# Performance work log

Hardware: AMD Instinct MI355X
Metric: run time of the kernel (lower is better)

Reference implementation:

```python
import jax, jax.numpy as jnp
import numpy as np

N_NODES = 50000
N_EDGES = 600000
N_GRAPHS = 128
D = 128
L = 3
OUT = 10
BN_EPS = 1e-5


def setup_inputs() -> dict:
    key = jax.random.key(0)
    ks = jax.random.split(key, 8)
    x = jax.random.normal(ks[0], (N_NODES, D), dtype=jnp.float32)
    edge_index = jax.random.randint(ks[1], (2, N_EDGES), 0, N_NODES, dtype=jnp.int64)
    batch = jnp.sort(jax.random.randint(ks[2], (N_NODES,), 0, N_GRAPHS, dtype=jnp.int64))
    s = 0.05
    return {
        "x": x,
        "edge_index": edge_index,
        "batch": batch,
        "convW1": jax.random.normal(ks[3], (L, D, D), dtype=jnp.float32) * s,
        "convb1": jnp.zeros((L, D), dtype=jnp.float32),
        "convg": jnp.ones((L, D), dtype=jnp.float32),
        "convbt": jnp.zeros((L, D), dtype=jnp.float32),
        "convW2": jax.random.normal(ks[4], (L, D, D), dtype=jnp.float32) * s,
        "convb2": jnp.zeros((L, D), dtype=jnp.float32),
        "mW1": jax.random.normal(ks[5], (D, D), dtype=jnp.float32) * s,
        "mb1": jnp.zeros((D,), dtype=jnp.float32),
        "mg": jnp.ones((D,), dtype=jnp.float32),
        "mbt": jnp.zeros((D,), dtype=jnp.float32),
        "mW2": jax.random.normal(ks[6], (D, OUT), dtype=jnp.float32) * s,
        "mb2": jnp.zeros((OUT,), dtype=jnp.float32),
    }


def _mlp(h, W1, b1, g, bt, W2, b2):
    # PyG MLP: Linear -> BatchNorm(eval: mean=0, var=1) -> ReLU -> Linear (plain last)
    inv = 1.0 / jnp.sqrt(1.0 + BN_EPS)
    h = h @ W1 + b1
    h = jnp.maximum(h * (inv * g) + bt, 0.0)
    return h @ W2 + b2


def reference(x, edge_index, batch, convW1, convb1, convg, convbt, convW2, convb2,
              mW1, mb1, mg, mbt, mW2, mb2):
    src, dst = edge_index[0], edge_index[1]
    for l in range(L):
        # GINConv (eps=0): nn(x + scatter-add of neighbor features)
        agg = jax.ops.segment_sum(x[src], dst, num_segments=N_NODES)  # [N, D]
        x = _mlp(x + agg, convW1[l], convb1[l], convg[l], convbt[l], convW2[l], convb2[l])
        x = jnp.maximum(x, 0.0)  # .relu() after conv
    pooled = jax.ops.segment_sum(x, batch, num_segments=N_GRAPHS)  # [G, D]
    return _mlp(pooled, mW1, mb1, mg, mbt, mW2, mb2)  # [G, OUT]
```

## Files before the change

### kernel.cpp

```cpp
#include <hip/hip_runtime.h>

#define N_NODES 50000
#define N_EDGES 600000
#define N_GRAPHS 128
#define DIM 128
#define NLAYERS 3
#define NOUT 10
#define ELLW 48
#define LSTRIDE 136
#define ZROW N_NODES

typedef unsigned short u16;
typedef __attribute__((ext_vector_type(8))) short bf16x8;
typedef __attribute__((ext_vector_type(4))) float f32x4;

__device__ __forceinline__ float bf2f(u16 v) {
    unsigned u = ((unsigned)v) << 16;
    return __builtin_bit_cast(float, u);
}
__device__ __forceinline__ u16 f2bf(float f) {
    unsigned u = __builtin_bit_cast(unsigned, f);
    u = u + 0x7fffu + ((u >> 16) & 1u);
    return (u16)(u >> 16);
}

__global__ void zero_small(int* __restrict__ deg, float* __restrict__ pooled) {
    int i = blockIdx.x * blockDim.x + threadIdx.x;
    if (i < N_NODES) deg[i] = 0;
    if (i < N_GRAPHS * DIM) pooled[i] = 0.f;
}

__global__ void prep_all(int* __restrict__ deg, int* __restrict__ ell,
                         const int* __restrict__ srcs, const int* __restrict__ dsts,
                         u16* __restrict__ xb, u16* __restrict__ bufA, u16* __restrict__ bufB,
                         const float* __restrict__ x, u16* __restrict__ Wswz,
                         const float* __restrict__ convW1, const float* __restrict__ convW2) {
    int i = blockIdx.x * blockDim.x + threadIdx.x;
    if (i < N_EDGES) {
        int d = dsts[i];
        int slot = atomicAdd(&deg[d], 1);
        if (slot < ELLW) ell[(size_t)d * ELLW + slot] = srcs[i];
    }
    if (i < DIM) {
        xb[(size_t)ZROW * DIM + i] = 0;
        bufA[(size_t)ZROW * DIM + i] = 0;
        bufB[(size_t)ZROW * DIM + i] = 0;
    }
    if (i < 6 * 16384) {
        int j = i & 7, lane = (i >> 3) & 63, cb = (i >> 9) & 7, kc = (i >> 12) & 3, w = i >> 14;
        int k = kc * 32 + ((lane >> 4) << 3) + j;
        int c = (cb << 4) + (lane & 15);
        const float* W = (w < 3) ? (convW1 + (size_t)w * 16384) : (convW2 + (size_t)(w - 3) * 16384);
        Wswz[i] = f2bf(W[k * DIM + c]);
    }
    if (i < N_NODES * DIM / 4) {
        float4 v = ((const float4*)x)[i];
        ushort4 o;
        o.x = f2bf(v.x); o.y = f2bf(v.y); o.z = f2bf(v.z); o.w = f2bf(v.w);
        ((ushort4*)xb)[i] = o;
    }
}

__global__ __launch_bounds__(256) void layer_fused(
    u16* __restrict__ out, const u16* __restrict__ x,
    const int* __restrict__ deg, const int* __restrict__ ell,
    const u16* __restrict__ W1f, const u16* __restrict__ W2f,
    const float* __restrict__ b1, const float* __restrict__ g1,
    const float* __restrict__ bt1, const float* __restrict__ b2) {
    __shared__ u16 A[16 * LSTRIDE];
    __shared__ u16 H[16 * LSTRIDE];
    const int tid = threadIdx.x;
    const int wv = tid >> 6;
    const int lane = tid & 63;
    const int row0 = blockIdx.x * 16;

    const size_t coff = (size_t)lane * 2;
    {
        const int r0 = wv << 2;
        int len[4];
        const int* ep[4];
        float ax[4], ay[4];
#pragma unroll
        for (int r = 0; r < 4; ++r) {
            const int grow = row0 + r0 + r;
            len[r] = min(deg[grow], ELLW);
            ep[r] = ell + (size_t)grow * ELLW;
            ushort2 self = *(const ushort2*)(x + (size_t)grow * DIM + coff);
            ax[r] = bf2f(self.x);
            ay[r] = bf2f(self.y);
        }
        const int maxlen = max(max(len[0], len[1]), max(len[2], len[3]));
        for (int j = 0; j < maxlen; j += 4) {
            int id[4][4];
#pragma unroll
            for (int r = 0; r < 4; ++r) {
                int4 e = *(const int4*)(ep[r] + j);
                id[r][0] = (j + 0 < len[r]) ? e.x : ZROW;
                id[r][1] = (j + 1 < len[r]) ? e.y : ZROW;
                id[r][2] = (j + 2 < len[r]) ? e.z : ZROW;
                id[r][3] = (j + 3 < len[r]) ? e.w : ZROW;
            }
#pragma unroll
            for (int r = 0; r < 4; ++r) {
                float px = 0.f, py = 0.f;
#pragma unroll
                for (int t = 0; t < 4; ++t) {
                    ushort2 v = *(const ushort2*)(x + (size_t)id[r][t] * DIM + coff);
                    px += bf2f(v.x);
                    py += bf2f(v.y);
                }
                ax[r] += px;
                ay[r] += py;
            }
        }
#pragma unroll
        for (int r = 0; r < 4; ++r) {
            ushort2 o;
            o.x = f2bf(ax[r]);
            o.y = f2bf(ay[r]);
            *(ushort2*)&A[(r0 + r) * LSTRIDE + lane * 2] = o;
        }
    }
    __syncthreads();

    const float inv = rsqrtf(1.f + 1e-5f);
    const int col0 = lane & 15;
    const int rbl = (lane >> 4) << 2;
    const int fragoff = (lane & 15) * LSTRIDE + ((lane >> 4) << 3);

    {
        f32x4 acc[2];
        acc[0] = (f32x4){0.f, 0.f, 0.f, 0.f};
        acc[1] = (f32x4){0.f, 0.f, 0.f, 0.f};
#pragma unroll
        for (int kc = 0; kc < 4; ++kc) {
            bf16x8 a = *(const bf16x8*)&A[fragoff + kc * 32];
#pragma unroll
            for (int m = 0; m < 2; ++m) {
                const int cb = (wv << 1) + m;
                bf16x8 bb = *(const bf16x8*)(W1f + ((((kc << 3) + cb) << 6 | lane) << 3));
                acc[m] = __builtin_amdgcn_mfma_f32_16x16x32_bf16(a, bb, acc[m], 0, 0, 0);
            }
        }
#pragma unroll
        for (int m = 0; m < 2; ++m) {
            const int c = (((wv << 1) + m) << 4) + col0;
            const float bias = b1[c];
            const float sg = inv * g1[c];
            const float st = bt1[c];
#pragma unroll
            for (int q = 0; q < 4; ++q) {
                float v = (acc[m][q] + bias) * sg + st;
                H[(rbl + q) * LSTRIDE + c] = f2bf(fmaxf(v, 0.f));
            }
        }
    }
    __syncthreads();

    {
        f32x4 acc[2];
        acc[0] = (f32x4){0.f, 0.f, 0.f, 0.f};
        acc[1] = (f32x4){0.f, 0.f, 0.f, 0.f};
#pragma unroll
        for (int kc = 0; kc < 4; ++kc) {
            bf16x8 a = *(const bf16x8*)&H[fragoff + kc * 32];
#pragma unroll
            for (int m = 0; m < 2; ++m) {
                const int cb = (wv << 1) + m;
                bf16x8 bb = *(const bf16x8*)(W2f + ((((kc << 3) + cb) << 6 | lane) << 3));
                acc[m] = __builtin_amdgcn_mfma_f32_16x16x32_bf16(a, bb, acc[m], 0, 0, 0);
            }
        }
#pragma unroll
        for (int m = 0; m < 2; ++m) {
            const int c = (((wv << 1) + m) << 4) + col0;
            const float bias = b2[c];
#pragma unroll
            for (int q = 0; q < 4; ++q) {
                float v = acc[m][q] + bias;
                A[(rbl + q) * LSTRIDE + c] = f2bf(fmaxf(v, 0.f));
            }
        }
    }
    __syncthreads();

    {
        const int r = tid >> 4;
        const int seg = tid & 15;
        uint4 v = *(const uint4*)&A[r * LSTRIDE + seg * 8];
        *(uint4*)(out + (size_t)(row0 + r) * DIM + seg * 8) = v;
    }
}

__global__ __launch_bounds__(256) void pool_partial(float* __restrict__ pooled,
                                                    const u16* __restrict__ x,
                                                    const int* __restrict__ batch) {
    const int chunk = (blockIdx.x * 256 + threadIdx.x) >> 6;
    const int lane = threadIdx.x & 63;
    const int beg = chunk * 16;
    if (beg >= N_NODES) return;
    const int end = min(beg + 16, N_NODES);
    const size_t coff = (size_t)lane * 2;

    float ax = 0.f, ay = 0.f;
    int curg = batch[beg];
    for (int n = beg; n < end; ++n) {
        int g = batch[n];
        if (g != curg) {
            atomicAdd(&pooled[(size_t)curg * DIM + coff], ax);
            atomicAdd(&pooled[(size_t)curg * DIM + coff + 1], ay);
            ax = 0.f; ay = 0.f; curg = g;
        }
        ushort2 v = *(const ushort2*)(x + (size_t)n * DIM + coff);
        ax += bf2f(v.x);
        ay += bf2f(v.y);
    }
    atomicAdd(&pooled[(size_t)curg * DIM + coff], ax);
    atomicAdd(&pooled[(size_t)curg * DIM + coff + 1], ay);
}

__global__ __launch_bounds__(128) void tail_mlp(float* __restrict__ out,
                                                const float* __restrict__ pooled,
                                                const float* __restrict__ mW1,
                                                const float* __restrict__ mb1,
                                                const float* __restrict__ mg,
                                                const float* __restrict__ mbt,
                                                const float* __restrict__ mW2,
                                                const float* __restrict__ mb2) {
    const int g = blockIdx.x;
    const int c = threadIdx.x;
    __shared__ float pl[DIM];
    __shared__ float hd[DIM];
    pl[c] = pooled[(size_t)g * DIM + c];
    __syncthreads();

    float s = 0.f;
#pragma unroll 4
    for (int k = 0; k < DIM; ++k) s += pl[k] * mW1[k * DIM + c];
    const float inv = rsqrtf(1.f + 1e-5f);
    s = (s + mb1[c]) * (inv * mg[c]) + mbt[c];
    hd[c] = fmaxf(s, 0.f);
    __syncthreads();

    if (c < NOUT) {
        float o = 0.f;
#pragma unroll 4
        for (int k = 0; k < DIM; ++k) o += hd[k] * mW2[k * NOUT + c];
        out[g * NOUT + c] = o + mb2[c];
    }
}

extern "C" void kernel_launch(void* const* d_in, const int* in_sizes, int n_in,
                              void* d_out, int out_size, void* d_ws, size_t ws_size,
                              hipStream_t stream) {
    const float* x      = (const float*)d_in[0];
    const int*   ei     = (const int*)d_in[1];
    const int*   batch  = (const int*)d_in[2];
    const float* convW1 = (const float*)d_in[3];
    const float* convb1 = (const float*)d_in[4];
    const float* convg  = (const float*)d_in[5];
    const float* convbt = (const float*)d_in[6];
    const float* convW2 = (const float*)d_in[7];
    const float* convb2 = (const float*)d_in[8];
    const float* mW1    = (const float*)d_in[9];
    const float* mb1    = (const float*)d_in[10];
    const float* mg     = (const float*)d_in[11];
    const float* mbt    = (const float*)d_in[12];
    const float* mW2    = (const float*)d_in[13];
    const float* mb2    = (const float*)d_in[14];
    float* out = (float*)d_out;

    const int* srcs = ei;
    const int* dsts = ei + N_EDGES;

    const size_t NFP = (size_t)(N_NODES + 1) * DIM;
    u16* xb0  = (u16*)d_ws;
    u16* bufA = xb0 + NFP;
    u16* bufB = bufA + NFP;
    u16* Wswz = bufB + NFP;
    float* pooled = (float*)(Wswz + 6 * 16384);
    int* deg = (int*)(pooled + N_GRAPHS * DIM);
    int* ell = deg + N_NODES;

    zero_small<<<(N_NODES + 255) / 256, 256, 0, stream>>>(deg, pooled);
    prep_all<<<(N_NODES * DIM / 4 + 255) / 256, 256, 0, stream>>>(
        deg, ell, srcs, dsts, xb0, bufA, bufB, x, Wswz, convW1, convW2);

    const int layerBlocks = N_NODES / 16;
    const u16* cur = xb0;
    u16* nxt = bufA;
    for (int l = 0; l < NLAYERS; ++l) {
        layer_fused<<<layerBlocks, 256, 0, stream>>>(
            nxt, cur, deg, ell,
            Wswz + (size_t)l * 16384, Wswz + (size_t)(3 + l) * 16384,
            convb1 + l * DIM, convg + l * DIM, convbt + l * DIM, convb2 + l * DIM);
        cur = nxt;
        nxt = (nxt == bufA) ? bufB : bufA;
    }

    const int poolBlocks = ((N_NODES + 15) / 16 * 64 + 255) / 256;
    pool_partial<<<poolBlocks, 256, 0, stream>>>(pooled, cur, batch);
    tail_mlp<<<N_GRAPHS, 128, 0, stream>>>(out, pooled, mW1, mb1, mg, mbt, mW2, mb2);
}
```

Before: 170.9 us.

## Store ELL indices as u16 and fuse sum-pooling into last layer

```diff
diff --git a/kernel.cpp b/kernel.cpp
--- a/kernel.cpp
+++ b/kernel.cpp
@@ -30,7 +30,7 @@
     if (i < N_GRAPHS * DIM) pooled[i] = 0.f;
 }
 
-__global__ void prep_all(int* __restrict__ deg, int* __restrict__ ell,
+__global__ void prep_all(int* __restrict__ deg, u16* __restrict__ ell,
                          const int* __restrict__ srcs, const int* __restrict__ dsts,
                          u16* __restrict__ xb, u16* __restrict__ bufA, u16* __restrict__ bufB,
                          const float* __restrict__ x, u16* __restrict__ Wswz,
@@ -39,7 +39,7 @@
     if (i < N_EDGES) {
         int d = dsts[i];
         int slot = atomicAdd(&deg[d], 1);
-        if (slot < ELLW) ell[(size_t)d * ELLW + slot] = srcs[i];
+        if (slot < ELLW) ell[(size_t)d * ELLW + slot] = (u16)srcs[i];
     }
     if (i < DIM) {
         xb[(size_t)ZROW * DIM + i] = 0;
@@ -61,24 +61,29 @@
     }
 }
 
+template <int POOL>
 __global__ __launch_bounds__(256) void layer_fused(
     u16* __restrict__ out, const u16* __restrict__ x,
-    const int* __restrict__ deg, const int* __restrict__ ell,
+    const int* __restrict__ deg, const u16* __restrict__ ell,
     const u16* __restrict__ W1f, const u16* __restrict__ W2f,
     const float* __restrict__ b1, const float* __restrict__ g1,
-    const float* __restrict__ bt1, const float* __restrict__ b2) {
+    const float* __restrict__ bt1, const float* __restrict__ b2,
+    const int* __restrict__ batch, float* __restrict__ pooled) {
     __shared__ u16 A[16 * LSTRIDE];
     __shared__ u16 H[16 * LSTRIDE];
+    __shared__ int gb[16];
     const int tid = threadIdx.x;
     const int wv = tid >> 6;
     const int lane = tid & 63;
     const int row0 = blockIdx.x * 16;
 
+    if (POOL && tid < 16) gb[tid] = batch[row0 + tid];
+
     const size_t coff = (size_t)lane * 2;
     {
         const int r0 = wv << 2;
         int len[4];
-        const int* ep[4];
+        const u16* ep[4];
         float ax[4], ay[4];
 #pragma unroll
         for (int r = 0; r < 4; ++r) {
@@ -94,11 +99,11 @@
             int id[4][4];
 #pragma unroll
             for (int r = 0; r < 4; ++r) {
-                int4 e = *(const int4*)(ep[r] + j);
-                id[r][0] = (j + 0 < len[r]) ? e.x : ZROW;
-                id[r][1] = (j + 1 < len[r]) ? e.y : ZROW;
-                id[r][2] = (j + 2 < len[r]) ? e.z : ZROW;
-                id[r][3] = (j + 3 < len[r]) ? e.w : ZROW;
+                ushort4 e = *(const ushort4*)(ep[r] + j);
+                id[r][0] = (j + 0 < len[r]) ? (int)e.x : ZROW;
+                id[r][1] = (j + 1 < len[r]) ? (int)e.y : ZROW;
+                id[r][2] = (j + 2 < len[r]) ? (int)e.z : ZROW;
+                id[r][3] = (j + 3 < len[r]) ? (int)e.w : ZROW;
             }
 #pragma unroll
             for (int r = 0; r < 4; ++r) {
@@ -184,39 +189,28 @@
     }
     __syncthreads();
 
-    {
+    if (!POOL) {
         const int r = tid >> 4;
         const int seg = tid & 15;
         uint4 v = *(const uint4*)&A[r * LSTRIDE + seg * 8];
         *(uint4*)(out + (size_t)(row0 + r) * DIM + seg * 8) = v;
-    }
-}
-
-__global__ __launch_bounds__(256) void pool_partial(float* __restrict__ pooled,
-                                                    const u16* __restrict__ x,
-                                                    const int* __restrict__ batch) {
-    const int chunk = (blockIdx.x * 256 + threadIdx.x) >> 6;
-    const int lane = threadIdx.x & 63;
-    const int beg = chunk * 16;
-    if (beg >= N_NODES) return;
-    const int end = min(beg + 16, N_NODES);
-    const size_t coff = (size_t)lane * 2;
-
-    float ax = 0.f, ay = 0.f;
-    int curg = batch[beg];
-    for (int n = beg; n < end; ++n) {
-        int g = batch[n];
-        if (g != curg) {
-            atomicAdd(&pooled[(size_t)curg * DIM + coff], ax);
-            atomicAdd(&pooled[(size_t)curg * DIM + coff + 1], ay);
-            ax = 0.f; ay = 0.f; curg = g;
-        }
-        ushort2 v = *(const ushort2*)(x + (size_t)n * DIM + coff);
-        ax += bf2f(v.x);
-        ay += bf2f(v.y);
-    }
-    atomicAdd(&pooled[(size_t)curg * DIM + coff], ax);
-    atomicAdd(&pooled[(size_t)curg * DIM + coff + 1], ay);
+    } else {
+        const int c = tid & 127;
+        const int rbeg = (tid >> 7) << 3;
+        float acc = 0.f;
+        int curg = gb[rbeg];
+#pragma unroll
+        for (int r = 0; r < 8; ++r) {
+            const int g = gb[rbeg + r];
+            if (g != curg) {
+                atomicAdd(&pooled[(size_t)curg * DIM + c], acc);
+                acc = 0.f;
+                curg = g;
+            }
+            acc += bf2f(A[(rbeg + r) * LSTRIDE + c]);
+        }
+        atomicAdd(&pooled[(size_t)curg * DIM + c], acc);
+    }
 }
 
 __global__ __launch_bounds__(128) void tail_mlp(float* __restrict__ out,
@@ -280,25 +274,22 @@
     u16* Wswz = bufB + NFP;
     float* pooled = (float*)(Wswz + 6 * 16384);
     int* deg = (int*)(pooled + N_GRAPHS * DIM);
-    int* ell = deg + N_NODES;
+    u16* ell = (u16*)(deg + N_NODES);
 
     zero_small<<<(N_NODES + 255) / 256, 256, 0, stream>>>(deg, pooled);
     prep_all<<<(N_NODES * DIM / 4 + 255) / 256, 256, 0, stream>>>(
         deg, ell, srcs, dsts, xb0, bufA, bufB, x, Wswz, convW1, convW2);
 
     const int layerBlocks = N_NODES / 16;
-    const u16* cur = xb0;
-    u16* nxt = bufA;
-    for (int l = 0; l < NLAYERS; ++l) {
-        layer_fused<<<layerBlocks, 256, 0, stream>>>(
-            nxt, cur, deg, ell,
-            Wswz + (size_t)l * 16384, Wswz + (size_t)(3 + l) * 16384,
-            convb1 + l * DIM, convg + l * DIM, convbt + l * DIM, convb2 + l * DIM);
-        cur = nxt;
-        nxt = (nxt == bufA) ? bufB : bufA;
-    }
-
-    const int poolBlocks = ((N_NODES + 15) / 16 * 64 + 255) / 256;
-    pool_partial<<<poolBlocks, 256, 0, stream>>>(pooled, cur, batch);
+    layer_fused<0><<<layerBlocks, 256, 0, stream>>>(
+        bufA, xb0, deg, ell, Wswz, Wswz + (size_t)3 * 16384,
+        convb1, convg, convbt, convb2, batch, pooled);
+    layer_fused<0><<<layerBlocks, 256, 0, stream>>>(
+        bufB, bufA, deg, ell, Wswz + (size_t)1 * 16384, Wswz + (size_t)4 * 16384,
+        convb1 + DIM, convg + DIM, convbt + DIM, convb2 + DIM, batch, pooled);
+    layer_fused<1><<<layerBlocks, 256, 0, stream>>>(
+        bufA , bufB, deg, ell, Wswz + (size_t)2 * 16384, Wswz + (size_t)5 * 16384,
+        convb1 + 2 * DIM, convg + 2 * DIM, convbt + 2 * DIM, convb2 + 2 * DIM, batch, pooled);
+
     tail_mlp<<<N_GRAPHS, 128, 0, stream>>>(out, pooled, mW1, mb1, mg, mbt, mW2, mb2);
 }
```

New measurement: 154.8 us. 1.1x faster.
